# Kernel optimization log

Hardware: AMD Instinct MI355X
Metric: run time of the kernel (lower is better)

The kernel has to match this reference:

```python
import jax, jax.numpy as jnp
import numpy as np

N, E = 50000, 800000
IN, H, D, C = 128, 4, 32, 40   # in_feats, heads, num_hiddens, n_classes
SLOPE, EPS = 0.2, 1e-5


def _glorot(key, shape, fan_in):
    return jax.random.normal(key, shape, dtype=jnp.float32) * (1.0 / np.sqrt(fan_in))


def setup_inputs() -> dict:
    key = jax.random.key(0)
    ks = jax.random.split(key, 24)
    inp = {
        "feat": jax.random.normal(ks[0], (N, IN), dtype=jnp.float32),
        "src": jax.random.randint(ks[1], (E,), 0, N, dtype=jnp.int32),
        "dst": jax.random.randint(ks[2], (E,), 0, N, dtype=jnp.int32),
    }
    # layer dims: (in_hidden, out_hidden)
    dims = [(IN, D), (H * D, D), (H * D, C)]
    k = 3
    for i, (fin, fout) in enumerate(dims):
        inp[f"Wc{i}"] = _glorot(ks[k], (fin, H * fout), fin); k += 1
        inp[f"al{i}"] = _glorot(ks[k], (H, fout), fout); k += 1
        inp[f"ar{i}"] = _glorot(ks[k], (H, fout), fout); k += 1
        inp[f"bc{i}"] = jnp.zeros((H * fout,), dtype=jnp.float32)
        inp[f"Wl{i}"] = _glorot(ks[k], (fin, H * fout), fin); k += 1
    for i in range(2):  # BN after layers 0 and 1
        inp[f"g{i}"] = jnp.ones((H * D,), dtype=jnp.float32)
        inp[f"b{i}"] = jnp.zeros((H * D,), dtype=jnp.float32)
    inp["bias_last"] = jnp.zeros((C,), dtype=jnp.float32)
    return inp


def _gat_layer(x, src, dst, Wc, al, ar, bc, Wl):
    n = x.shape[0]
    h, d = al.shape
    z = (x @ Wc).reshape(n, h, d)                      # [N,H,D]
    el = jnp.sum(z * al, axis=-1)                      # [N,H]
    er = jnp.sum(z * ar, axis=-1)                      # [N,H]
    e = jax.nn.leaky_relu(el[src] + er[dst], SLOPE)    # [E,H]
    m = jax.ops.segment_max(e, dst, num_segments=n)    # edge-softmax (stable)
    ex = jnp.exp(e - m[dst])
    s = jax.ops.segment_sum(ex, dst, num_segments=n)
    alpha = ex / jnp.where(s == 0, 1.0, s)[dst]        # [E,H]
    agg = jax.ops.segment_sum(alpha[:, :, None] * z[src], dst, num_segments=n)
    conv = agg + bc.reshape(h, d)
    lin = (x @ Wl).reshape(n, h, d)
    return conv + lin                                   # [N,H,D]


def _bn(x, g, b):
    mu = jnp.mean(x, axis=0)
    var = jnp.mean((x - mu) ** 2, axis=0)
    return (x - mu) * jax.lax.rsqrt(var + EPS) * g + b


def reference(feat, src, dst,
              Wc0, al0, ar0, bc0, Wl0,
              Wc1, al1, ar1, bc1, Wl1,
              Wc2, al2, ar2, bc2, Wl2,
              g0, b0, g1, b1, bias_last):
    h = feat
    h = _gat_layer(h, src, dst, Wc0, al0, ar0, bc0, Wl0)
    h = jax.nn.relu(_bn(h.reshape(h.shape[0], -1), g0, b0))
    h = _gat_layer(h, src, dst, Wc1, al1, ar1, bc1, Wl1)
    h = jax.nn.relu(_bn(h.reshape(h.shape[0], -1), g1, b1))
    h = _gat_layer(h, src, dst, Wc2, al2, ar2, bc2, Wl2)
    h = h.mean(axis=1)                                  # mean over heads -> [N,C]
    return h + bias_last
```

## Files before the change

### kernel.cpp

```cpp
#include <hip/hip_runtime.h>
#include <hip/hip_bf16.h>

typedef __hip_bfloat16 bf16;
typedef __attribute__((ext_vector_type(8))) short short8;
typedef __attribute__((ext_vector_type(4))) float f32x4;

__device__ __forceinline__ float b2f(bf16 x) { return __bfloat162float(x); }
__device__ __forceinline__ float bits2f(unsigned short u) {
    return __uint_as_float(((unsigned)u) << 16);
}
__device__ __forceinline__ float ldw(const void* p, int i, int m) {
    return m ? ((const float*)p)[i] : b2f(((const bf16*)p)[i]);
}

__global__ __launch_bounds__(256) void k_zero_probe(int* __restrict__ counts, float* __restrict__ bn0,
                                                    float* __restrict__ bn1, int n,
                                                    const void* __restrict__ feat, int* __restrict__ mode) {
    int t = blockIdx.x * 256 + threadIdx.x;
    if (t < n) counts[t] = 0;
    if (t < 256) { bn0[t] = 0.f; bn1[t] = 0.f; }
    if (blockIdx.x == 0 && threadIdx.x < 64) {
        const bf16* p = (const bf16*)feat;
        int lane = threadIdx.x;
        float m = 0.f;
        for (int i = lane; i < 2048; i += 64) {
            float v = fabsf(b2f(p[2 * i]));
            if (!(v < 1e30f)) v = 1e30f;
            m = fmaxf(m, v);
        }
        #pragma unroll
        for (int off = 32; off > 0; off >>= 1) m = fmaxf(m, __shfl_xor(m, off, 64));
        if (lane == 0) *mode = (m > 1e8f) ? 1 : 0;
    }
}

struct SmallDesc { const void* src; float* dst; int n; };
struct SmallArgs { SmallDesc d[14]; };
__global__ __launch_bounds__(256) void k_prep(const void* __restrict__ Wc0, const void* __restrict__ Wl0,
                                              const void* __restrict__ Wc1, const void* __restrict__ Wl1,
                                              const void* __restrict__ Wc2, const void* __restrict__ Wl2,
                                              bf16* __restrict__ Wt0, bf16* __restrict__ Wt1,
                                              bf16* __restrict__ Wt2, SmallArgs sa,
                                              const int* __restrict__ mode) {
    int m = *mode;
    int bx = blockIdx.x;
    if (bx < 416) {
        int t = bx * 256 + threadIdx.x;
        const void* Wc; const void* Wl; bf16* Wt; int HC, c2, k;
        if (t < 32768)       { Wc = Wc0; Wl = Wl0; Wt = Wt0; HC = 128; c2 = t & 255; k = t >> 8; }
        else if (t < 65536)  { t -= 32768; Wc = Wc1; Wl = Wl1; Wt = Wt1; HC = 128; c2 = t & 255; k = t >> 8; }
        else                 { t -= 65536; Wc = Wc2; Wl = Wl2; Wt = Wt2; HC = 160; c2 = t % 320; k = t / 320; }
        float v = (c2 < HC) ? ldw(Wc, k * HC + c2, m) : ldw(Wl, k * HC + c2 - HC, m);
        int tile = c2 >> 4, c16 = c2 & 15, kg = k >> 5, q = (k >> 3) & 3, j = k & 7;
        Wt[tile * 2048 + kg * 512 + c16 * 32 + q * 8 + j] = __float2bfloat16(v);
    } else {
        #pragma unroll 1
        for (int i = 0; i < 14; i++) {
            const SmallDesc sd = sa.d[i];
            for (int t = threadIdx.x; t < sd.n; t += 256) sd.dst[t] = ldw(sd.src, t, m);
        }
    }
}


__global__ __launch_bounds__(256) void k_hist(const int* __restrict__ dst, int* __restrict__ counts, int e) {
    int t = blockIdx.x * 256 + threadIdx.x;
    if (t < e) atomicAdd(&counts[dst[t]], 1);
}

__global__ __launch_bounds__(1024) void k_scan(const int* __restrict__ counts, int* __restrict__ row_ptr,
                                               int* __restrict__ cursor, int n) {
    __shared__ int wsum[16];
    __shared__ int carry_s;
    int lane = threadIdx.x & 63, w = threadIdx.x >> 6;
    if (threadIdx.x == 0) carry_s = 0;
    __syncthreads();
    for (int base = 0; base < n; base += 16384) {
        int i0 = base + (int)threadIdx.x * 16;
        int v[16];
        #pragma unroll
        for (int jb = 0; jb < 16; jb += 4) {
            int idx = i0 + jb;
            if (idx + 3 < n) {
                int4 t4 = *(const int4*)(counts + idx);
                v[jb] = t4.x; v[jb + 1] = t4.y; v[jb + 2] = t4.z; v[jb + 3] = t4.w;
            } else {
                #pragma unroll
                for (int q = 0; q < 4; q++) v[jb + q] = (idx + q < n) ? counts[idx + q] : 0;
            }
        }
        int pre[16]; int tot = 0;
        #pragma unroll
        for (int j = 0; j < 16; j++) { pre[j] = tot; tot += v[j]; }
        int x = tot;
        #pragma unroll
        for (int off = 1; off < 64; off <<= 1) {
            int t = __shfl_up(x, off, 64);
            if (lane >= off) x += t;
        }
        if (lane == 63) wsum[w] = x;
        __syncthreads();
        if (w == 0 && lane < 16) {
            int s = wsum[lane];
            #pragma unroll
            for (int off = 1; off < 16; off <<= 1) {
                int t = __shfl_up(s, off, 64);
                if (lane >= off) s += t;
            }
            wsum[lane] = s;
        }
        __syncthreads();
        int carry = carry_s;
        int woff = (w == 0) ? 0 : wsum[w - 1];
        int excl = carry + woff + x - tot;
        #pragma unroll
        for (int jb = 0; jb < 16; jb += 4) {
            int idx = i0 + jb;
            if (idx + 3 < n) {
                int4 rp = {excl + pre[jb], excl + pre[jb + 1], excl + pre[jb + 2], excl + pre[jb + 3]};
                *(int4*)(row_ptr + idx) = rp;
                *(int4*)(cursor + idx) = rp;
            } else {
                #pragma unroll
                for (int q = 0; q < 4; q++)
                    if (idx + q < n) { row_ptr[idx + q] = excl + pre[jb + q]; cursor[idx + q] = excl + pre[jb + q]; }
            }
        }
        __syncthreads();
        if (threadIdx.x == 0) carry_s = carry + wsum[15];
        __syncthreads();
    }
    if (threadIdx.x == 0) row_ptr[n] = carry_s;
}

__global__ __launch_bounds__(256) void k_scatter(const int* __restrict__ src, const int* __restrict__ dst,
                                                 int* __restrict__ cursor, int* __restrict__ ssrc,
                                                 int e, int rpb) {
    int range = blockIdx.x & 7;
    int t = (blockIdx.x >> 3) * 256 + threadIdx.x;
    if (t < e) {
        int d = dst[t];
        if ((int)((unsigned)d / (unsigned)rpb) == range) {
            int idx = atomicAdd(&cursor[d], 1);
            ssrc[idx] = src[t];
        }
    }
}

template <int HC, int CT, int AMODE, bool FELR>
__global__ __launch_bounds__(256) void k_gemm_mfma(const void* __restrict__ Av, const int* __restrict__ mode,
                                                   const bf16* __restrict__ Wt,
                                                   bf16* __restrict__ Zh, float* __restrict__ Lin,
                                                   const float* __restrict__ alp, const float* __restrict__ arp,
                                                   float* __restrict__ elp, float* __restrict__ erp,
                                                   const float* __restrict__ bnsum, const float* __restrict__ bnsq,
                                                   const float* __restrict__ gg, const float* __restrict__ bb,
                                                   float invn, int n) {
    constexpr int TW = CT * 16;
    constexpr int TS = (TW + 8 > 136) ? (TW + 8) : 136;
    __shared__ short lds_a[64 * TS];
    __shared__ float lds_bn[256];
    int tid = threadIdx.x;
    int wv = tid >> 6, lane = tid & 63;
    int quad = lane >> 4, m16 = lane & 15;
    int row0 = blockIdx.x * 64 + wv * 16;
    int row0b = blockIdx.x * 64;
    int col0 = blockIdx.y * TW;
    if constexpr (AMODE == 2) {
        if (tid < 128) {
            float mu = bnsum[tid] * invn;
            float var = bnsq[tid] * invn - mu * mu;
            float sc = rsqrtf(var + 1e-5f) * gg[tid];
            lds_bn[tid] = sc;
            lds_bn[128 + tid] = bb[tid] - mu * sc;
        }
        __syncthreads();
    }
    bool af32 = false;
    if constexpr (AMODE == 1) af32 = (*mode != 0);
    #pragma unroll
    for (int i = 0; i < 4; i++) {
        int f = i * 256 + tid;
        int row = f >> 4, c8 = f & 15;
        int arow = row0b + row; if (arow >= n) arow = n - 1;
        union { bf16 h[8]; short8 s; } u;
        if (AMODE == 2 || (AMODE == 1 && af32)) {
            const float4* ap = (const float4*)((const float*)Av + (size_t)arow * 128 + c8 * 8);
            float4 g0v = ap[0], g1v = ap[1];
            float vals[8] = {g0v.x, g0v.y, g0v.z, g0v.w, g1v.x, g1v.y, g1v.z, g1v.w};
            if constexpr (AMODE == 2) {
                int c0 = c8 * 8;
                #pragma unroll
                for (int j = 0; j < 8; j++) {
                    float r = vals[j] * lds_bn[c0 + j] + lds_bn[128 + c0 + j];
                    vals[j] = r > 0.f ? r : 0.f;
                }
            }
            #pragma unroll
            for (int j = 0; j < 8; j++) u.h[j] = __float2bfloat16(vals[j]);
        } else {
            u.s = *(const short8*)((const bf16*)Av + (size_t)arow * 128 + c8 * 8);
        }
        *(short8*)(&lds_a[row * 136 + c8 * 8]) = u.s;
    }
    __syncthreads();
    f32x4 acc[CT] = {};
    const short8* Bp = (const short8*)Wt;
    int lr = wv * 16 + m16;
    int ctb = blockIdx.y * CT;
    #pragma unroll
    for (int k8 = 0; k8 < 16; k8 += 4) {
        short8 a = *(const short8*)(&lds_a[lr * 136 + (k8 + quad) * 8]);
        #pragma unroll
        for (int c = 0; c < CT; c++) {
            short8 b = Bp[(size_t)(ctb + c) * 256 + k8 * 16 + m16 * 4 + quad];
            acc[c] = __builtin_amdgcn_mfma_f32_16x16x32_bf16(a, b, acc[c], 0, 0, 0);
        }
    }
    if constexpr (FELR && HC == 128) {
        if (blockIdx.y == 0) {
            float a0[4], a1[4], r0[4], r1[4];
            #pragma unroll
            for (int h = 0; h < 4; h++) {
                a0[h] = alp[h * 32 + m16]; a1[h] = alp[h * 32 + 16 + m16];
                r0[h] = arp[h * 32 + m16]; r1[h] = arp[h * 32 + 16 + m16];
            }
            #pragma unroll
            for (int reg = 0; reg < 4; reg++) {
                float eh[8];
                #pragma unroll
                for (int h = 0; h < 4; h++) {
                    eh[h]     = acc[2 * h][reg] * a0[h] + acc[2 * h + 1][reg] * a1[h];
                    eh[4 + h] = acc[2 * h][reg] * r0[h] + acc[2 * h + 1][reg] * r1[h];
                }
                #pragma unroll
                for (int off = 1; off < 16; off <<= 1) {
                    #pragma unroll
                    for (int k = 0; k < 8; k++) eh[k] += __shfl_xor(eh[k], off, 64);
                }
                int r = row0 + quad * 4 + reg;
                float vl = (m16 & 2) ? ((m16 & 1) ? eh[3] : eh[2]) : ((m16 & 1) ? eh[1] : eh[0]);
                float vr = (m16 & 2) ? ((m16 & 1) ? eh[7] : eh[6]) : ((m16 & 1) ? eh[5] : eh[4]);
                if (r < n && m16 < 4) { elp[(size_t)r * 4 + m16] = vl; erp[(size_t)r * 4 + m16] = vr; }
            }
        }
    }
    if constexpr (FELR && HC == 160) {
        if (blockIdx.y == 0) {
            float alv[10], arv[10];
            #pragma unroll
            for (int c = 0; c < 10; c++) { alv[c] = alp[c * 16 + m16]; arv[c] = arp[c * 16 + m16]; }
            #pragma unroll
            for (int reg = 0; reg < 4; reg++) {
                float eh[8] = {0.f, 0.f, 0.f, 0.f, 0.f, 0.f, 0.f, 0.f};
                #pragma unroll
                for (int c = 0; c < 10; c++) {
                    int col = c * 16 + m16;
                    float zl = acc[c][reg] * alv[c];
                    float zr = acc[c][reg] * arv[c];
                    bool h0 = col < 40, h1 = (col >= 40) & (col < 80);
                    bool h2 = (col >= 80) & (col < 120), h3 = col >= 120;
                    eh[0] += h0 ? zl : 0.f; eh[1] += h1 ? zl : 0.f;
                    eh[2] += h2 ? zl : 0.f; eh[3] += h3 ? zl : 0.f;
                    eh[4] += h0 ? zr : 0.f; eh[5] += h1 ? zr : 0.f;
                    eh[6] += h2 ? zr : 0.f; eh[7] += h3 ? zr : 0.f;
                }
                #pragma unroll
                for (int off = 1; off < 16; off <<= 1) {
                    #pragma unroll
                    for (int k = 0; k < 8; k++) eh[k] += __shfl_xor(eh[k], off, 64);
                }
                int r = row0 + quad * 4 + reg;
                float vl = (m16 & 2) ? ((m16 & 1) ? eh[3] : eh[2]) : ((m16 & 1) ? eh[1] : eh[0]);
                float vr = (m16 & 2) ? ((m16 & 1) ? eh[7] : eh[6]) : ((m16 & 1) ? eh[5] : eh[4]);
                if (r < n && m16 < 4) { elp[(size_t)r * 4 + m16] = vl; erp[(size_t)r * 4 + m16] = vr; }
            }
        }
    }
    if (blockIdx.y == 0) {
        __syncthreads();
        #pragma unroll
        for (int c = 0; c < CT; c++) {
            #pragma unroll
            for (int reg = 0; reg < 4; reg++) {
                int rrel = wv * 16 + quad * 4 + reg;
                lds_a[rrel * TS + c * 16 + m16] = (short)__bfloat16_as_ushort(__float2bfloat16(acc[c][reg]));
            }
        }
        __syncthreads();
        constexpr int CH = TW / 8;
        for (int f = tid; f < 64 * CH; f += 256) {
            int row = f / CH, c8 = f % CH;
            int arow = row0b + row;
            if (arow < n)
                *(short8*)(Zh + (size_t)arow * HC + c8 * 8) = *(const short8*)(&lds_a[row * TS + c8 * 8]);
        }
    } else {
        #pragma unroll
        for (int c = 0; c < CT; c++) {
            int gc = col0 + c * 16 + m16;
            #pragma unroll
            for (int reg = 0; reg < 4; reg++) {
                int r = row0 + quad * 4 + reg;
                if (r >= n) continue;
                Lin[(size_t)r * HC + gc - HC] = acc[c][reg];
            }
        }
    }
}

template <int HC, int D, bool LAST>
__global__ __launch_bounds__(256, 8) void k_gather(const int* __restrict__ row_ptr, const int* __restrict__ ssrc,
                                                   const float* __restrict__ el, const float* __restrict__ er,
                                                   const float* __restrict__ bc, const bf16* __restrict__ Z,
                                                   float* __restrict__ Y, const float* __restrict__ bias,
                                                   float* __restrict__ out, int n) {
    constexpr int DPL = HC / 16;
    constexpr int UN = (DPL == 8) ? 4 : 2;
    int node = (int)((blockIdx.x * blockDim.x + threadIdx.x) >> 6);
    int lane = threadIdx.x & 63;
    if (node >= n) return;
    int qi = lane >> 4;
    int t16 = lane & 15;
    int hq = t16 >> 2;
    int beg = row_ptr[node], end = row_ptr[node + 1];
    float4 er4 = ((const float4*)er)[node];
    const float4* el4p = (const float4*)el;
    const bf16* Zt = Z + t16 * DPL;
    float acc[DPL];
    #pragma unroll
    for (int k = 0; k < DPL; k++) acc[k] = 0.f;
    float ss = 0.f;
    for (int base = beg; base < end; base += 64) {
        int idx = base + lane;
        bool valid = idx < end;
        int s_my = valid ? ssrc[idx] : 0;
        float4 e4 = el4p[s_my];
        float x0 = e4.x + er4.x; x0 = x0 > 0.f ? x0 : 0.2f * x0;
        float x1 = e4.y + er4.y; x1 = x1 > 0.f ? x1 : 0.2f * x1;
        float x2 = e4.z + er4.z; x2 = x2 > 0.f ? x2 : 0.2f * x2;
        float x3 = e4.w + er4.w; x3 = x3 > 0.f ? x3 : 0.2f * x3;
        float w0 = valid ? __expf(x0) : 0.f;
        float w1 = valid ? __expf(x1) : 0.f;
        float w2 = valid ? __expf(x2) : 0.f;
        float w3 = valid ? __expf(x3) : 0.f;
        int cnt = end - base; if (cnt > 64) cnt = 64;
        int iters = (cnt + 3) >> 2;
        for (int j = 0; j < iters; j += UN) {
            int sv[UN]; float gv[UN];
            #pragma unroll
            for (int f = 0; f < UN; f++) {
                int sl = qi + ((j + f) << 2);
                sv[f] = __shfl(s_my, sl, 64);
                float a0 = __shfl(w0, sl, 64);
                float a1 = __shfl(w1, sl, 64);
                float a2 = __shfl(w2, sl, 64);
                float a3 = __shfl(w3, sl, 64);
                gv[f] = (hq & 2) ? ((hq & 1) ? a3 : a2) : ((hq & 1) ? a1 : a0);
                ss += gv[f];
            }
            if constexpr (DPL == 8) {
                short8 z[UN];
                #pragma unroll
                for (int f = 0; f < UN; f++) z[f] = *(const short8*)(Zt + (size_t)sv[f] * HC);
                #pragma unroll
                for (int f = 0; f < UN; f++) {
                    #pragma unroll
                    for (int k = 0; k < 8; k++)
                        acc[k] += gv[f] * bits2f((unsigned short)z[f][k]);
                }
            } else {
                __hip_bfloat162 z[UN][DPL / 2];
                #pragma unroll
                for (int f = 0; f < UN; f++) {
                    const __hip_bfloat162* z2 = (const __hip_bfloat162*)(Zt + (size_t)sv[f] * HC);
                    #pragma unroll
                    for (int k2 = 0; k2 < DPL / 2; k2++) z[f][k2] = z2[k2];
                }
                #pragma unroll
                for (int f = 0; f < UN; f++) {
                    #pragma unroll
                    for (int k2 = 0; k2 < DPL / 2; k2++) {
                        acc[2 * k2]     += gv[f] * b2f(z[f][k2].x);
                        acc[2 * k2 + 1] += gv[f] * b2f(z[f][k2].y);
                    }
                }
            }
        }
    }
    #pragma unroll
    for (int k = 0; k < DPL; k++) {
        acc[k] += __shfl_xor(acc[k], 16, 64);
        acc[k] += __shfl_xor(acc[k], 32, 64);
    }
    ss += __shfl_xor(ss, 16, 64);
    ss += __shfl_xor(ss, 32, 64);
    float inv = (end > beg) ? 1.f / ss : 0.f;
    if constexpr (!LAST) {
        if ((lane & 48) == 0) {
            float* yr = Y + (size_t)node * HC + t16 * DPL;
            const float* bcr = bc + t16 * DPL;
            #pragma unroll
            for (int k = 0; k < DPL; k++) yr[k] += acc[k] * inv + bcr[k];
        }
    } else {
        float yv[DPL];
        const float* lr = Y + (size_t)node * HC + t16 * DPL;
        const float* bcr = bc + t16 * DPL;
        #pragma unroll
        for (int k = 0; k < DPL; k++) yv[k] = acc[k] * inv + bcr[k] + lr[k];
        #pragma unroll
        for (int k = 0; k < DPL; k++) {
            yv[k] += __shfl_xor(yv[k], 4, 64);
            yv[k] += __shfl_xor(yv[k], 8, 64);
        }
        if (lane < 4) {
            float* orow = out + (size_t)node * 40 + t16 * DPL;
            const float* br = bias + t16 * DPL;
            #pragma unroll
            for (int k = 0; k < DPL; k++) orow[k] = 0.25f * yv[k] + br[k];
        }
    }
}

__global__ __launch_bounds__(256) void k_bn_stats(const float* __restrict__ Y, float* __restrict__ sum,
                                                  float* __restrict__ sumsq, int n) {
    __shared__ float4 lds_s[8][32];
    __shared__ float4 lds_q[8][32];
    int t = threadIdx.x;
    int q = t & 31, g = t >> 5;
    const float4* Y4 = (const float4*)Y;
    float4 s = {0.f, 0.f, 0.f, 0.f}, ss = {0.f, 0.f, 0.f, 0.f};
    const int stride = 128 * 8;
    int r = blockIdx.x * 8 + g;
    for (; r + stride < n; r += 2 * stride) {
        float4 v0 = Y4[(size_t)r * 32 + q];
        float4 v1 = Y4[(size_t)(r + stride) * 32 + q];
        s.x += v0.x; s.y += v0.y; s.z += v0.z; s.w += v0.w;
        ss.x += v0.x * v0.x; ss.y += v0.y * v0.y; ss.z += v0.z * v0.z; ss.w += v0.w * v0.w;
        s.x += v1.x; s.y += v1.y; s.z += v1.z; s.w += v1.w;
        ss.x += v1.x * v1.x; ss.y += v1.y * v1.y; ss.z += v1.z * v1.z; ss.w += v1.w * v1.w;
    }
    if (r < n) {
        float4 v = Y4[(size_t)r * 32 + q];
        s.x += v.x; s.y += v.y; s.z += v.z; s.w += v.w;
        ss.x += v.x * v.x; ss.y += v.y * v.y; ss.z += v.z * v.z; ss.w += v.w * v.w;
    }
    lds_s[g][q] = s; lds_q[g][q] = ss;
    __syncthreads();
    if (t < 32) {
        float4 S = lds_s[0][t], Q = lds_q[0][t];
        #pragma unroll
        for (int g2 = 1; g2 < 8; g2++) {
            float4 a = lds_s[g2][t], b = lds_q[g2][t];
            S.x += a.x; S.y += a.y; S.z += a.z; S.w += a.w;
            Q.x += b.x; Q.y += b.y; Q.z += b.z; Q.w += b.w;
        }
        atomicAdd(&sum[4 * t + 0], S.x); atomicAdd(&sum[4 * t + 1], S.y);
        atomicAdd(&sum[4 * t + 2], S.z); atomicAdd(&sum[4 * t + 3], S.w);
        atomicAdd(&sumsq[4 * t + 0], Q.x); atomicAdd(&sumsq[4 * t + 1], Q.y);
        atomicAdd(&sumsq[4 * t + 2], Q.z); atomicAdd(&sumsq[4 * t + 3], Q.w);
    }
}


extern "C" void kernel_launch(void* const* d_in, const int* in_sizes, int n_in,
                              void* d_out, int out_size, void* d_ws, size_t ws_size,
                              hipStream_t stream) {
    (void)n_in; (void)out_size; (void)ws_size;
    const int N = in_sizes[0] / 128;
    const int E = in_sizes[1];

    const int* src = (const int*)d_in[1];
    const int* dst = (const int*)d_in[2];
    float* out = (float*)d_out;

    char* p = (char*)d_ws;
    auto carve = [&](size_t bytes) {
        void* q = (void*)p;
        p += (bytes + 255) & ~(size_t)255;
        return q;
    };
    int*   mode    = (int*)  carve(256);
    bf16*  zh      = (bf16*) carve((size_t)N * 160 * 2);
    float* P0      = (float*)carve((size_t)N * 160 * 4);
    float* P1      = (float*)carve((size_t)N * 128 * 4);
    float* el      = (float*)carve((size_t)N * 4 * 4);
    float* er      = (float*)carve((size_t)N * 4 * 4);
    float* bn0     = (float*)carve(256 * 4);
    float* bn1     = (float*)carve(256 * 4);
    int*   counts  = (int*)  carve((size_t)N * 4);
    int*   row_ptr = (int*)  carve((size_t)(N + 1) * 4);
    int*   cursor  = (int*)  carve((size_t)N * 4);
    int*   ssrc    = (int*)  carve((size_t)E * 4);
    bf16*  Wt0     = (bf16*) carve((size_t)2 * 128 * 128 * 2);
    bf16*  Wt1     = (bf16*) carve((size_t)2 * 128 * 128 * 2);
    bf16*  Wt2     = (bf16*) carve((size_t)2 * 160 * 128 * 2);
    const int small_idx[14] = {4, 5, 6, 9, 10, 11, 14, 15, 16, 18, 19, 20, 21, 22};
    float* Wsm[14];
    for (int j = 0; j < 14; j++) Wsm[j] = (float*)carve((size_t)in_sizes[small_idx[j]] * 4);

    const float* alw[3] = {Wsm[0], Wsm[3], Wsm[6]};
    const float* arw[3] = {Wsm[1], Wsm[4], Wsm[7]};
    const float* bcw[3] = {Wsm[2], Wsm[5], Wsm[8]};
    const float* g0 = Wsm[9];
    const float* b0 = Wsm[10];
    const float* g1 = Wsm[11];
    const float* b1 = Wsm[12];
    const float* bias_last = Wsm[13];

    const int EB = (E + 255) / 256;
    const int GB_ROWS = (N + 63) / 64;
    const int NODE_BLK = (N + 3) / 4;
    const float invn = 1.f / (float)N;
    const int RPB = (N + 7) / 8;

    k_zero_probe<<<(N + 255) / 256, 256, 0, stream>>>(counts, bn0, bn1, N, d_in[0], mode);
    SmallArgs sa;
    for (int j = 0; j < 14; j++) sa.d[j] = SmallDesc{d_in[small_idx[j]], Wsm[j], in_sizes[small_idx[j]]};
    k_prep<<<417, 256, 0, stream>>>(d_in[3], d_in[7], d_in[8], d_in[12], d_in[13], d_in[17],
                                    Wt0, Wt1, Wt2, sa, mode);
    k_hist<<<EB, 256, 0, stream>>>(dst, counts, E);
    k_scan<<<1, 1024, 0, stream>>>(counts, row_ptr, cursor, N);
    k_scatter<<<8 * EB, 256, 0, stream>>>(src, dst, cursor, ssrc, E, RPB);

    k_gemm_mfma<128, 8, 1, true><<<dim3(GB_ROWS, 2), 256, 0, stream>>>(
        d_in[0], mode, Wt0, zh, P0, alw[0], arw[0], el, er,
        nullptr, nullptr, nullptr, nullptr, 0.f, N);
    k_gather<128, 32, false><<<NODE_BLK, 256, 0, stream>>>(row_ptr, ssrc, el, er, bcw[0], zh,
                                                           P0, nullptr, nullptr, N);
    k_bn_stats<<<128, 256, 0, stream>>>(P0, bn0, bn0 + 128, N);

    k_gemm_mfma<128, 8, 2, true><<<dim3(GB_ROWS, 2), 256, 0, stream>>>(
        P0, mode, Wt1, zh, P1, alw[1], arw[1], el, er,
        bn0, bn0 + 128, g0, b0, invn, N);
    k_gather<128, 32, false><<<NODE_BLK, 256, 0, stream>>>(row_ptr, ssrc, el, er, bcw[1], zh,
                                                           P1, nullptr, nullptr, N);
    k_bn_stats<<<128, 256, 0, stream>>>(P1, bn1, bn1 + 128, N);

    k_gemm_mfma<160, 10, 2, true><<<dim3(GB_ROWS, 2), 256, 0, stream>>>(
        P1, mode, Wt2, zh, P0, alw[2], arw[2], el, er,
        bn1, bn1 + 128, g1, b1, invn, N);
    k_gather<160, 40, true><<<NODE_BLK, 256, 0, stream>>>(row_ptr, ssrc, el, er, bcw[2], zh,
                                                          P0, bias_last, out, N);
}
```

Baseline: 464.8 us.

## Shard layer-0/1 gather by head across blocks with head-major el layout

Adds a k_gather_h kernel that splits each node's aggregation into four head shards handled by separate blocks. Each wave gathers 16 edges per round and reads 64 contiguous bytes per source row, and el is written head-major so a shard reads it contiguously. The aim is more parallelism and less per-lane shuffle and select overhead in the 128-wide layers. In exchange it launches four times as many blocks, reads row_ptr and ssrc four times, and may lose cache locality on Z rows. The last layer still uses the old gather, which now reads el with the row-major layout even though the 160-wide path's el store is not shown changing.

```diff
diff --git a/kernel.cpp b/kernel.cpp
--- a/kernel.cpp
+++ b/kernel.cpp
@@ -241,7 +241,7 @@
                 int r = row0 + quad * 4 + reg;
                 float vl = (m16 & 2) ? ((m16 & 1) ? eh[3] : eh[2]) : ((m16 & 1) ? eh[1] : eh[0]);
                 float vr = (m16 & 2) ? ((m16 & 1) ? eh[7] : eh[6]) : ((m16 & 1) ? eh[5] : eh[4]);
-                if (r < n && m16 < 4) { elp[(size_t)r * 4 + m16] = vl; erp[(size_t)r * 4 + m16] = vr; }
+                if (r < n && m16 < 4) { elp[(size_t)m16 * n + r] = vl; erp[(size_t)r * 4 + m16] = vr; }
             }
         }
     }
@@ -306,6 +306,60 @@
                 Lin[(size_t)r * HC + gc - HC] = acc[c][reg];
             }
         }
+    }
+}
+
+__global__ __launch_bounds__(256, 8) void k_gather_h(const int* __restrict__ row_ptr,
+                                                     const int* __restrict__ ssrc,
+                                                     const float* __restrict__ elt,
+                                                     const float* __restrict__ er,
+                                                     const float* __restrict__ bc, const bf16* __restrict__ Z,
+                                                     float* __restrict__ Y, int n) {
+    int shard = blockIdx.x & 3;
+    int wv = threadIdx.x >> 6, lane = threadIdx.x & 63;
+    int node = ((blockIdx.x >> 2) << 2) + wv;
+    if (node >= n) return;
+    int slot = lane >> 2, li = lane & 3;
+    int beg = row_ptr[node], end = row_ptr[node + 1];
+    float er_s = er[node * 4 + shard];
+    const float* el_s = elt + (size_t)shard * n;
+    const bf16* Zs = Z + shard * 32 + li * 8;
+    float acc[8];
+    #pragma unroll
+    for (int k = 0; k < 8; k++) acc[k] = 0.f;
+    float ss = 0.f;
+    for (int base = beg; base < end; base += 64) {
+        int idx = base + lane;
+        bool valid = idx < end;
+        int s_my = valid ? ssrc[idx] : 0;
+        float x = el_s[s_my] + er_s;
+        x = x > 0.f ? x : 0.2f * x;
+        float w_my = valid ? __expf(x) : 0.f;
+        int cnt = end - base; if (cnt > 64) cnt = 64;
+        int rounds = (cnt + 15) >> 4;
+        for (int j = 0; j < rounds; j++) {
+            int sl = slot + (j << 4);
+            int s = __shfl(s_my, sl, 64);
+            float w = __shfl(w_my, sl, 64);
+            ss += w;
+            short8 z8 = *(const short8*)(Zs + (size_t)s * 128);
+            #pragma unroll
+            for (int k = 0; k < 8; k++)
+                acc[k] += w * bits2f((unsigned short)z8[k]);
+        }
+    }
+    #pragma unroll
+    for (int off = 4; off < 64; off <<= 1) {
+        #pragma unroll
+        for (int k = 0; k < 8; k++) acc[k] += __shfl_xor(acc[k], off, 64);
+        ss += __shfl_xor(ss, off, 64);
+    }
+    float inv = (end > beg) ? 1.f / ss : 0.f;
+    if (lane < 4) {
+        float* yr = Y + (size_t)node * 128 + shard * 32 + li * 8;
+        const float* bcr = bc + shard * 32 + li * 8;
+        #pragma unroll
+        for (int k = 0; k < 8; k++) yr[k] += acc[k] * inv + bcr[k];
     }
 }
 
@@ -359,31 +413,19 @@
                 gv[f] = (hq & 2) ? ((hq & 1) ? a3 : a2) : ((hq & 1) ? a1 : a0);
                 ss += gv[f];
             }
-            if constexpr (DPL == 8) {
-                short8 z[UN];
-                #pragma unroll
-                for (int f = 0; f < UN; f++) z[f] = *(const short8*)(Zt + (size_t)sv[f] * HC);
-                #pragma unroll
-                for (int f = 0; f < UN; f++) {
-                    #pragma unroll
-                    for (int k = 0; k < 8; k++)
-                        acc[k] += gv[f] * bits2f((unsigned short)z[f][k]);
-                }
-            } else {
-                __hip_bfloat162 z[UN][DPL / 2];
-                #pragma unroll
-                for (int f = 0; f < UN; f++) {
-                    const __hip_bfloat162* z2 = (const __hip_bfloat162*)(Zt + (size_t)sv[f] * HC);
-                    #pragma unroll
-                    for (int k2 = 0; k2 < DPL / 2; k2++) z[f][k2] = z2[k2];
-                }
-                #pragma unroll
-                for (int f = 0; f < UN; f++) {
-                    #pragma unroll
-                    for (int k2 = 0; k2 < DPL / 2; k2++) {
-                        acc[2 * k2]     += gv[f] * b2f(z[f][k2].x);
-                        acc[2 * k2 + 1] += gv[f] * b2f(z[f][k2].y);
-                    }
+            __hip_bfloat162 z[UN][DPL / 2];
+            #pragma unroll
+            for (int f = 0; f < UN; f++) {
+                const __hip_bfloat162* z2 = (const __hip_bfloat162*)(Zt + (size_t)sv[f] * HC);
+                #pragma unroll
+                for (int k2 = 0; k2 < DPL / 2; k2++) z[f][k2] = z2[k2];
+            }
+            #pragma unroll
+            for (int f = 0; f < UN; f++) {
+                #pragma unroll
+                for (int k2 = 0; k2 < DPL / 2; k2++) {
+                    acc[2 * k2]     += gv[f] * b2f(z[f][k2].x);
+                    acc[2 * k2 + 1] += gv[f] * b2f(z[f][k2].y);
                 }
             }
         }
@@ -527,15 +569,13 @@
     k_gemm_mfma<128, 8, 1, true><<<dim3(GB_ROWS, 2), 256, 0, stream>>>(
         d_in[0], mode, Wt0, zh, P0, alw[0], arw[0], el, er,
         nullptr, nullptr, nullptr, nullptr, 0.f, N);
-    k_gather<128, 32, false><<<NODE_BLK, 256, 0, stream>>>(row_ptr, ssrc, el, er, bcw[0], zh,
-                                                           P0, nullptr, nullptr, N);
+    k_gather_h<<<NODE_BLK * 4, 256, 0, stream>>>(row_ptr, ssrc, el, er, bcw[0], zh, P0, N);
     k_bn_stats<<<128, 256, 0, stream>>>(P0, bn0, bn0 + 128, N);
 
     k_gemm_mfma<128, 8, 2, true><<<dim3(GB_ROWS, 2), 256, 0, stream>>>(
         P0, mode, Wt1, zh, P1, alw[1], arw[1], el, er,
         bn0, bn0 + 128, g0, b0, invn, N);
-    k_gather<128, 32, false><<<NODE_BLK, 256, 0, stream>>>(row_ptr, ssrc, el, er, bcw[1], zh,
-                                                           P1, nullptr, nullptr, N);
+    k_gather_h<<<NODE_BLK * 4, 256, 0, stream>>>(row_ptr, ssrc, el, er, bcw[1], zh, P1, N);
     k_bn_stats<<<128, 256, 0, stream>>>(P1, bn1, bn1 + 128, N);
 
     k_gemm_mfma<160, 10, 2, true><<<dim3(GB_ROWS, 2), 256, 0, stream>>>(
```

Result: slower. 569.5 us (+22.5%).
